# Performance work log

Measured on AMD Instinct MI355X. Metric: run time of the kernel, lower is better.

## Reference

```python
import jax, jax.numpy as jnp
import numpy as np
from jax import lax

B, S, D, H, K = 2, 2048, 1024, 16, 3  # batch, seq, embed, heads, conv kernel
DEPTH = D // H


def silu(x):
    return x * jax.nn.sigmoid(x)


def sep_conv1d(x, dw, pw, b):
    """Keras SeparableConv1D, padding='same', activation=silu.
    x: [B,S,C]; dw: [K,1,C] depthwise kernel; pw: [C,F] pointwise; b: [F]."""
    C = x.shape[-1]
    y = lax.conv_general_dilated(
        x, dw, window_strides=(1,), padding='SAME',
        dimension_numbers=('NWC', 'WIO', 'NWC'), feature_group_count=C)
    y = jnp.einsum('bsc,cf->bsf', y, pw) + b
    return silu(y)


def setup_inputs() -> dict:
    key = jax.random.key(0)
    ks = jax.random.split(key, 20)
    sc = 1.0 / np.sqrt(D)
    inp = {
        'v': jax.random.normal(ks[0], (B, S, D), jnp.float32),
        'k': jax.random.normal(ks[1], (B, S, D), jnp.float32),
        'q': jax.random.normal(ks[2], (B, S, D), jnp.float32),
        'mask': jax.random.randint(ks[3], (B, 1, 1, S), 0, 2, jnp.int32),
        # Dense wq/wk/wv (SiLU)
        'wq_w': jax.random.normal(ks[4], (D, D), jnp.float32) * sc,
        'wq_b': jnp.zeros((D,), jnp.float32),
        'wk_w': jax.random.normal(ks[5], (D, D), jnp.float32) * sc,
        'wk_b': jnp.zeros((D,), jnp.float32),
        'wv_w': jax.random.normal(ks[6], (D, D), jnp.float32) * sc,
        'wv_b': jnp.zeros((D,), jnp.float32),
        # SeparableConv1D params (depthwise [K,1,D], pointwise [D,D], bias [D])
        'dwq': jax.random.normal(ks[7], (K, 1, D), jnp.float32) * 0.1,
        'pwq': jax.random.normal(ks[8], (D, D), jnp.float32) * sc,
        'bq': jnp.zeros((D,), jnp.float32),
        'dwk': jax.random.normal(ks[9], (K, 1, D), jnp.float32) * 0.1,
        'pwk': jax.random.normal(ks[10], (D, D), jnp.float32) * sc,
        'bk': jnp.zeros((D,), jnp.float32),
        'dwv': jax.random.normal(ks[11], (K, 1, D), jnp.float32) * 0.1,
        'pwv': jax.random.normal(ks[12], (D, D), jnp.float32) * sc,
        'bv': jnp.zeros((D,), jnp.float32),
        # output Dense (SiLU)
        'wo_w': jax.random.normal(ks[13], (D, D), jnp.float32) * sc,
        'wo_b': jnp.zeros((D,), jnp.float32),
    }
    return inp


def reference(v, k, q, mask, wq_w, wq_b, wk_w, wk_b, wv_w, wv_b,
              dwq, pwq, bq, dwk, pwk, bk, dwv, pwv, bv, wo_w, wo_b):
    # Dense projections with SiLU
    qp = silu(q @ wq_w + wq_b)
    kp = silu(k @ wk_w + wk_b)
    vp = silu(v @ wv_w + wv_b)
    # SeparableConv1D enhancements (SiLU)
    qc = sep_conv1d(qp, dwq, pwq, bq)
    kc = sep_conv1d(kp, dwk, pwk, bk)
    vc = sep_conv1d(vp, dwv, pwv, bv)
    # split heads -> [B,H,S,depth]
    def split(x):
        return x.reshape(B, S, H, DEPTH).transpose(0, 2, 1, 3)
    qh, kh, vh = split(qc), split(kc), split(vc)
    # scaled dot-product attention with additive mask penalty
    logits = jnp.einsum('bhqd,bhkd->bhqk', qh, kh) / jnp.sqrt(jnp.float32(DEPTH))
    logits = logits + mask.astype(jnp.float32) * -1e9
    attn = jax.nn.softmax(logits, axis=-1)
    out = jnp.einsum('bhqk,bhkd->bhqd', attn, vh)
    out = out.transpose(0, 2, 1, 3).reshape(B, S, D)
    return silu(out @ wo_w + wo_b)
```

## Files before the change

kernel.cpp:

```cpp
#include <hip/hip_runtime.h>
#include <hip/hip_fp16.h>
#include <math.h>

#define BB 2
#define SS 2048
#define DD 1024
#define HH 16
#define MTOT (BB*SS)

typedef _Float16 f16;
typedef _Float16 f16x4 __attribute__((ext_vector_type(4)));
typedef _Float16 f16x8 __attribute__((ext_vector_type(8)));
typedef float    f32x4 __attribute__((ext_vector_type(4)));

#define KSCALE 0.1803368801111204f

__device__ __forceinline__ float silu_f(float x) {
    return x / (1.0f + __expf(-x));
}

__device__ __forceinline__ void gload16(void* lds, const void* g) {
    __builtin_amdgcn_global_load_lds(
        (const __attribute__((address_space(1))) unsigned*)g,
        (__attribute__((address_space(3))) unsigned*)lds, 16, 0, 0);
}

__global__ __launch_bounds__(256) void prep(
    const float* __restrict__ q, const float* __restrict__ k, const float* __restrict__ v,
    f16* __restrict__ x0, f16* __restrict__ x1, f16* __restrict__ x2,
    const float* __restrict__ w0, const float* __restrict__ w1, const float* __restrict__ w2,
    const float* __restrict__ w3, const float* __restrict__ w4, const float* __restrict__ w5,
    const float* __restrict__ w6, f16* __restrict__ wt,
    const int* __restrict__ mask, int* __restrict__ uidx, int* __restrict__ ucnt)
{
    __shared__ float ts[64][65];
    const int gid = blockIdx.x;
    const int t = threadIdx.x;

    if (gid < 6144) {
        const int z = gid >> 11;
        const float* src = z == 0 ? q : z == 1 ? k : v;
        f16* dst = z == 0 ? x0 : z == 1 ? x1 : x2;
        const size_t i8 = ((size_t)(gid & 2047) * 256 + t) * 8;
        const float4 a = *(const float4*)(src + i8);
        const float4 b = *(const float4*)(src + i8 + 4);
        f16x8 h = {(f16)a.x,(f16)a.y,(f16)a.z,(f16)a.w,(f16)b.x,(f16)b.y,(f16)b.z,(f16)b.w};
        *(f16x8*)(dst + i8) = h;
    } else if (gid < 7936) {
        const int w = gid - 6144;
        const int z = w >> 8;
        const int rem = w & 255;
        const int bn = (rem & 15) << 6, bk = (rem >> 4) << 6;
        const float* src;
        switch (z) {
            case 0: src = w0; break; case 1: src = w1; break;
            case 2: src = w2; break; case 3: src = w3; break;
            case 4: src = w4; break; case 5: src = w5; break;
            default: src = w6; break;
        }
        f16* dst = wt + ((size_t)z << 20);
        #pragma unroll
        for (int i = 0; i < 4; ++i) {
            const int fid = t + (i << 8);
            const int r = fid >> 4, c4 = (fid & 15) << 2;
            const float4 v4 = *(const float4*)(src + (size_t)(bk + r) * 1024 + bn + c4);
            ts[r][c4 + 0] = v4.x; ts[r][c4 + 1] = v4.y;
            ts[r][c4 + 2] = v4.z; ts[r][c4 + 3] = v4.w;
        }
        __syncthreads();
        #pragma unroll
        for (int i = 0; i < 4; ++i) {
            const int fid = t + (i << 8);
            const int nr = fid >> 4, k4 = (fid & 15) << 2;
            f16x4 h = { (f16)ts[k4 + 0][nr], (f16)ts[k4 + 1][nr],
                        (f16)ts[k4 + 2][nr], (f16)ts[k4 + 3][nr] };
            *(f16x4*)(dst + (size_t)(bn + nr) * 1024 + bk + k4) = h;
        }
    } else {
        int* ps = (int*)ts;
        const int b = gid - 7936;
        int f[8]; int cnt = 0;
        const int base = b * SS + t * 8;
        #pragma unroll
        for (int j = 0; j < 8; ++j) { f[j] = (mask[base + j] == 0); cnt += f[j]; }
        ps[t] = cnt;
        __syncthreads();
        for (int off = 1; off < 256; off <<= 1) {
            const int pv = (t >= off) ? ps[t - off] : 0;
            __syncthreads();
            ps[t] += pv;
            __syncthreads();
        }
        int pos = ps[t] - cnt;
        #pragma unroll
        for (int j = 0; j < 8; ++j)
            if (f[j]) uidx[b * SS + pos++] = t * 8 + j;
        const int total = ps[255];
        const int pad = (total + 63) & ~63;
        for (int j = total + t; j < pad; j += 256) uidx[b * SS + j] = 0;
        if (t == 0) { ucnt[b * 2] = total; ucnt[b * 2 + 1] = pad; }
    }
}

__global__ __launch_bounds__(256) void dwconv3g(
    const f16* __restrict__ p0, const f16* __restrict__ p1, const f16* __restrict__ p2,
    const float* __restrict__ w0, const float* __restrict__ w1, const float* __restrict__ w2,
    f16* __restrict__ o0, f16* __restrict__ o1, f16* __restrict__ o2)
{
    const int z = blockIdx.y;
    const f16* x = z == 0 ? p0 : z == 1 ? p1 : p2;
    const float* dw = z == 0 ? w0 : z == 1 ? w1 : w2;
    f16* y = z == 0 ? o0 : z == 1 ? o1 : o2;
    const size_t i8 = ((size_t)blockIdx.x * 256 + threadIdx.x) * 8;
    const int c = (int)(i8 % DD);
    const int s = (int)((i8 / DD) % SS);
    const f16x8 xc = *(const f16x8*)(x + i8);
    float acc[8];
    #pragma unroll
    for (int j = 0; j < 8; ++j) acc[j] = (float)xc[j] * dw[DD + c + j];
    if (s > 0) {
        const f16x8 xm = *(const f16x8*)(x + i8 - DD);
        #pragma unroll
        for (int j = 0; j < 8; ++j) acc[j] = fmaf((float)xm[j], dw[c + j], acc[j]);
    }
    if (s < SS - 1) {
        const f16x8 xp = *(const f16x8*)(x + i8 + DD);
        #pragma unroll
        for (int j = 0; j < 8; ++j) acc[j] = fmaf((float)xp[j], dw[2 * DD + c + j], acc[j]);
    }
    f16x8 o;
    #pragma unroll
    for (int j = 0; j < 8; ++j) o[j] = (f16)acc[j];
    *(f16x8*)(y + i8) = o;
}

struct GArg { const f16* A; const f16* W; const float* b; void* C; float scale; };

template<int OUTF32>
__global__ __launch_bounds__(256) void gemm_f16(GArg g0, GArg g1, GArg g2)
{
    __shared__ f16 As[128 * 64];
    __shared__ f16 Bs[128 * 64];

    const GArg ga = blockIdx.z == 0 ? g0 : blockIdx.z == 1 ? g1 : g2;
    const int t = threadIdx.x, l = t & 63, wv = t >> 6;
    const int lr = l & 15, lg = l >> 4;
    const int wr = wv >> 1, wc = wv & 1;

    const int bid = blockIdx.y * 8 + blockIdx.x;
    const int sw = (bid & 7) * 32 + (bid >> 3);
    const int brow = (sw >> 3) << 7, bcol = (sw & 7) << 7;

    const int srow = l >> 3;
    const int schk = (l & 7) ^ (l >> 3);
    const f16* Abase = ga.A + (size_t)(brow + wv * 32 + srow) * 1024 + schk * 8;
    const f16* Bbase = ga.W + (size_t)(bcol + wv * 32 + srow) * 1024 + schk * 8;

    f32x4 acc[4][4];
    #pragma unroll
    for (int m = 0; m < 4; ++m)
        #pragma unroll
        for (int n = 0; n < 4; ++n) acc[m][n] = (f32x4){0.f, 0.f, 0.f, 0.f};

    for (int kt = 0; kt < 16; ++kt) {
        const int k0 = kt << 6;
        #pragma unroll
        for (int j = 0; j < 4; ++j) {
            gload16(As + (wv * 4 + j) * 512, Abase + (size_t)j * 8 * 1024 + k0);
            gload16(Bs + (wv * 4 + j) * 512, Bbase + (size_t)j * 8 * 1024 + k0);
        }
        __syncthreads();

        #pragma unroll
        for (int kk = 0; kk < 2; ++kk) {
            f16x8 af[4], bf[4];
            #pragma unroll
            for (int m = 0; m < 4; ++m) {
                const int row = (wr << 6) + (m << 4) + lr;
                const int off = row * 128 + ((((kk << 6) | (lg << 4))) ^ ((lr & 7) << 4));
                af[m] = *(const f16x8*)((const char*)As + off);
            }
            #pragma unroll
            for (int n = 0; n < 4; ++n) {
                const int row = (wc << 6) + (n << 4) + lr;
                const int off = row * 128 + ((((kk << 6) | (lg << 4))) ^ ((lr & 7) << 4));
                bf[n] = *(const f16x8*)((const char*)Bs + off);
            }
            #pragma unroll
            for (int m = 0; m < 4; ++m)
                #pragma unroll
                for (int n = 0; n < 4; ++n)
                    acc[m][n] = __builtin_amdgcn_mfma_f32_16x16x32_f16(af[m], bf[n], acc[m][n], 0, 0, 0);
        }
        __syncthreads();
    }

    float bv[4];
    #pragma unroll
    for (int n = 0; n < 4; ++n) bv[n] = ga.b[bcol + (wc << 6) + (n << 4) + lr];
    #pragma unroll
    for (int m = 0; m < 4; ++m)
        #pragma unroll
        for (int n = 0; n < 4; ++n)
            #pragma unroll
            for (int i = 0; i < 4; ++i) {
                const int row = brow + (wr << 6) + (m << 4) + (lg << 2) + i;
                const int col = bcol + (wc << 6) + (n << 4) + lr;
                const float o = silu_f(acc[m][n][i] + bv[n]) * ga.scale;
                if (OUTF32) ((float*)ga.C)[(size_t)row * 1024 + col] = o;
                else        ((f16*)ga.C)[(size_t)row * 1024 + col] = (f16)o;
            }
}

__global__ __launch_bounds__(512) void gemm256(GArg g0, GArg g1, GArg g2)
{
    __shared__ f16 As[256 * 64];
    __shared__ f16 Bs[128 * 64];

    const GArg ga = blockIdx.z == 0 ? g0 : blockIdx.z == 1 ? g1 : g2;
    const int t = threadIdx.x, l = t & 63, wv = t >> 6;
    const int lr = l & 15, lg = l >> 4;
    const int wm = wv >> 1, wn = wv & 1;

    const int bid = blockIdx.y * 8 + blockIdx.x;
    const int sw = (bid & 7) * 16 + (bid >> 3);
    const int brow = (sw >> 3) << 8;
    const int bcol = (sw & 7) << 7;

    const int srow = l >> 3;
    const int schk = (l & 7) ^ (l >> 3);
    const f16* Abase = ga.A + (size_t)(brow + wv * 32 + srow) * 1024 + schk * 8;
    const f16* Bbase = ga.W + (size_t)(bcol + wv * 16 + srow) * 1024 + schk * 8;

    f32x4 acc[4][4];
    #pragma unroll
    for (int m = 0; m < 4; ++m)
        #pragma unroll
        for (int n = 0; n < 4; ++n) acc[m][n] = (f32x4){0.f, 0.f, 0.f, 0.f};

    for (int kt = 0; kt < 16; ++kt) {
        const int k0 = kt << 6;
        #pragma unroll
        for (int j = 0; j < 4; ++j)
            gload16(As + (wv * 4 + j) * 512, Abase + (size_t)j * 8 * 1024 + k0);
        #pragma unroll
        for (int j = 0; j < 2; ++j)
            gload16(Bs + (wv * 2 + j) * 512, Bbase + (size_t)j * 8 * 1024 + k0);
        __syncthreads();

        #pragma unroll
        for (int kk = 0; kk < 2; ++kk) {
            f16x8 af[4], bf[4];
            #pragma unroll
            for (int m = 0; m < 4; ++m) {
                const int row = (wm << 6) + (m << 4) + lr;
                const int off = row * 128 + ((((kk << 6) | (lg << 4))) ^ ((lr & 7) << 4));
                af[m] = *(const f16x8*)((const char*)As + off);
            }
            #pragma unroll
            for (int n = 0; n < 4; ++n) {
                const int row = (wn << 6) + (n << 4) + lr;
                const int off = row * 128 + ((((kk << 6) | (lg << 4))) ^ ((lr & 7) << 4));
                bf[n] = *(const f16x8*)((const char*)Bs + off);
            }
            #pragma unroll
            for (int m = 0; m < 4; ++m)
                #pragma unroll
                for (int n = 0; n < 4; ++n)
                    acc[m][n] = __builtin_amdgcn_mfma_f32_16x16x32_f16(af[m], bf[n], acc[m][n], 0, 0, 0);
        }
        __syncthreads();
    }

    float bv[4];
    #pragma unroll
    for (int n = 0; n < 4; ++n) bv[n] = ga.b[bcol + (wn << 6) + (n << 4) + lr];
    #pragma unroll
    for (int m = 0; m < 4; ++m)
        #pragma unroll
        for (int n = 0; n < 4; ++n)
            #pragma unroll
            for (int i = 0; i < 4; ++i) {
                const int row = brow + (wm << 6) + (m << 4) + (lg << 2) + i;
                const int col = bcol + (wn << 6) + (n << 4) + lr;
                const float o = silu_f(acc[m][n][i] + bv[n]) * ga.scale;
                ((f16*)ga.C)[(size_t)row * 1024 + col] = (f16)o;
            }
}

__global__ __launch_bounds__(512) void attn_f16(
    const f16* __restrict__ Q, const f16* __restrict__ Kf,
    const f16* __restrict__ Vf, const int* __restrict__ uidx,
    const int* __restrict__ ucnt, f16* __restrict__ O)
{
    __shared__ f16 Ks[2 * 64 * 64];
    __shared__ f16 Vt[2 * 64 * 64];
    __shared__ f16 Pw[8 * 16 * 64];
    __shared__ int uix[2048];

    const int t = threadIdx.x;
    const int l = t & 63, wv = t >> 6;
    const int lr = l & 15, lg = l >> 4;

    const int bid = blockIdx.x;
    const int sw = (bid & 7) * 64 + (bid >> 3);
    const int qb = (sw & 15) << 7;
    const int h  = (sw >> 4) & 15;
    const int b  = sw >> 8;

    const int cnt = ucnt[b * 2];
    const int pad = ucnt[b * 2 + 1];

    const int srow = l >> 3;
    const int schk = (l & 7) ^ (l >> 3);

    const int bkv = (t & 15) << 2;
    const int bnv = (t >> 4) << 2;

    for (int j = t; j < 2048; j += 512) uix[j] = uidx[b * SS + j];

    const size_t bbase = (size_t)b * SS;
    const size_t qrow = bbase + qb + (wv << 4) + lr;
    const f16x8 aq0 = *(const f16x8*)(Q + qrow * DD + h * 64 + (lg << 3));
    const f16x8 aq1 = *(const f16x8*)(Q + qrow * DD + h * 64 + 32 + (lg << 3));

    float m_i[4], l_i[4];
    f32x4 acc[4];
    #pragma unroll
    for (int i = 0; i < 4; ++i) { m_i[i] = -1e30f; l_i[i] = 0.f; }
    #pragma unroll
    for (int n = 0; n < 4; ++n) acc[n] = (f32x4){0.f, 0.f, 0.f, 0.f};

    const int rdswz = (lr & 7) << 4;
    const int poff = (wv << 11) + lr * 128;

    __syncthreads();

#define PROCESS(TB, KT) do {                                                  \
    const int kb = (TB) * 8192;                                               \
    f16x8 bk0[4], bk1[4];                                                     \
    _Pragma("unroll")                                                         \
    for (int n = 0; n < 4; ++n) {                                             \
        const int row = (n << 4) + lr;                                        \
        bk0[n] = *(const f16x8*)((const char*)Ks + kb + row * 128 + (((lg << 4)) ^ rdswz));        \
        bk1[n] = *(const f16x8*)((const char*)Ks + kb + row * 128 + (((64) | (lg << 4)) ^ rdswz)); \
    }                                                                         \
    const bool full = ((KT) + 64 <= cnt);                                     \
    f32x4 s[4];                                                               \
    __builtin_amdgcn_s_setprio(1);                                            \
    _Pragma("unroll")                                                         \
    for (int n = 0; n < 4; ++n) {                                             \
        f32x4 z = (f32x4){0.f, 0.f, 0.f, 0.f};                                \
        z = __builtin_amdgcn_mfma_f32_16x16x32_f16(aq0, bk0[n], z, 0, 0, 0);  \
        z = __builtin_amdgcn_mfma_f32_16x16x32_f16(aq1, bk1[n], z, 0, 0, 0);  \
        if (full) {                                                           \
            _Pragma("unroll")                                                 \
            for (int i = 0; i < 4; ++i) s[n][i] = z[i];                       \
        } else {                                                              \
            const bool valid = ((KT) + (n << 4) + lr) < cnt;                  \
            _Pragma("unroll")                                                 \
            for (int i = 0; i < 4; ++i) s[n][i] = valid ? z[i] : -1e30f;      \
        }                                                                     \
    }                                                                         \
    __builtin_amdgcn_s_setprio(0);                                            \
    float pm[4];                                                              \
    _Pragma("unroll")                                                         \
    for (int i = 0; i < 4; ++i)                                               \
        pm[i] = fmaxf(fmaxf(s[0][i], s[1][i]), fmaxf(s[2][i], s[3][i]));      \
    float g = pm[0] - m_i[0];                                                 \
    _Pragma("unroll")                                                         \
    for (int i = 1; i < 4; ++i) g = fmaxf(g, pm[i] - m_i[i]);                 \
    if (!__all(g <= 8.0f)) {                 \
        float sc[4];                                                          \
        _Pragma("unroll")                                                     \
        for (int i = 0; i < 4; ++i) {                                         \
            float pr = pm[i];                                                 \
            pr = fmaxf(pr, __shfl_xor(pr, 1));                                \
            pr = fmaxf(pr, __shfl_xor(pr, 2));                                \
            pr = fmaxf(pr, __shfl_xor(pr, 4));                                \
            pr = fmaxf(pr, __shfl_xor(pr, 8));                                \
            const float mn = fmaxf(m_i[i], pr);                               \
            sc[i] = exp2f(m_i[i] - mn);                                       \
            m_i[i] = mn;                                                      \
            l_i[i] *= sc[i];                                                  \
        }                                                                     \
        _Pragma("unroll")                                                     \
        for (int n = 0; n < 4; ++n)                                           \
            _Pragma("unroll")                                                 \
            for (int i = 0; i < 4; ++i) acc[n][i] *= sc[i];                   \
    }                                                                         \
    _Pragma("unroll")                                                         \
    for (int n = 0; n < 4; ++n)                                               \
        _Pragma("unroll")                                                     \
        for (int i = 0; i < 4; ++i) {                                         \
            const float p = exp2f(s[n][i] - m_i[i]);      \
            l_i[i] += p;                                                      \
            const int row = (lg << 2) + i;                                    \
            const int off = (wv << 11) + row * 128 +                          \
                            ((((n << 4) + lr) * 2) ^ ((row & 7) << 4));       \
            *(f16*)((char*)Pw + off) = (f16)p;                                \
        }                                                                     \
    {                                                                         \
        const f16x8 pa0 = *(const f16x8*)((const char*)Pw + poff + (((lg << 4)) ^ rdswz));        \
        const f16x8 pa1 = *(const f16x8*)((const char*)Pw + poff + (((64) | (lg << 4)) ^ rdswz)); \
        __builtin_amdgcn_s_setprio(1);                                        \
        _Pragma("unroll")                                                     \
        for (int n = 0; n < 4; ++n) {                                         \
            const int row = (n << 4) + lr;                                    \
            const f16x8 bv0 = *(const f16x8*)((const char*)Vt + kb + row * 128 + (((lg << 4)) ^ rdswz));        \
            const f16x8 bv1 = *(const f16x8*)((const char*)Vt + kb + row * 128 + (((64) | (lg << 4)) ^ rdswz)); \
            acc[n] = __builtin_amdgcn_mfma_f32_16x16x32_f16(pa0, bv0, acc[n], 0, 0, 0);  \
            acc[n] = __builtin_amdgcn_mfma_f32_16x16x32_f16(pa1, bv1, acc[n], 0, 0, 0);  \
        }                                                                     \
        __builtin_amdgcn_s_setprio(0);                                        \
    }                                                                         \
} while (0)

    for (int kt = 0; kt < pad; kt += 128) {
        const bool two = (kt + 64) < pad;
        {
            const int krow0 = uix[kt + wv * 8 + srow];
            gload16(Ks + wv * 512, Kf + (bbase + krow0) * DD + h * 64 + schk * 8);
            if (two) {
                const int krow1 = uix[kt + 64 + wv * 8 + srow];
                gload16(Ks + 4096 + wv * 512, Kf + (bbase + krow1) * DD + h * 64 + schk * 8);
            }
        }
        if (t < 256) {
            const int nhalf = two ? 2 : 1;
            for (int half = 0; half < nhalf; ++half) {
                f16x4 vl[4];
                #pragma unroll
                for (int r = 0; r < 4; ++r) {
                    const int vrow = uix[kt + half * 64 + bkv + r];
                    vl[r] = *(const f16x4*)(Vf + (bbase + vrow) * DD + h * 64 + bnv);
                }
                #pragma unroll
                for (int j = 0; j < 4; ++j) {
                    f16x4 h4 = { vl[0][j], vl[1][j], vl[2][j], vl[3][j] };
                    const int row = bnv + j;
                    const int off = half * 8192 + row * 128 + ((bkv * 2) ^ ((row & 7) << 4));
                    *(f16x4*)((char*)Vt + off) = h4;
                }
            }
        }
        __syncthreads();

        PROCESS(0, kt);
        if (two) PROCESS(1, kt + 64);

        __syncthreads();
    }
#undef PROCESS

    #pragma unroll
    for (int i = 0; i < 4; ++i) {
        l_i[i] += __shfl_xor(l_i[i], 1);
        l_i[i] += __shfl_xor(l_i[i], 2);
        l_i[i] += __shfl_xor(l_i[i], 4);
        l_i[i] += __shfl_xor(l_i[i], 8);
    }
    #pragma unroll
    for (int n = 0; n < 4; ++n)
        #pragma unroll
        for (int i = 0; i < 4; ++i) {
            const size_t row = bbase + qb + (wv << 4) + (lg << 2) + i;
            O[row * DD + h * 64 + (n << 4) + lr] = (f16)(acc[n][i] / l_i[i]);
        }
}

extern "C" void kernel_launch(void* const* d_in, const int* in_sizes, int n_in,
                              void* d_out, int out_size, void* d_ws, size_t ws_size,
                              hipStream_t stream) {
    const float* v    = (const float*)d_in[0];
    const float* k    = (const float*)d_in[1];
    const float* q    = (const float*)d_in[2];
    const int*   mask = (const int*)  d_in[3];
    const float* wq_w = (const float*)d_in[4];
    const float* wq_b = (const float*)d_in[5];
    const float* wk_w = (const float*)d_in[6];
    const float* wk_b = (const float*)d_in[7];
    const float* wv_w = (const float*)d_in[8];
    const float* wv_b = (const float*)d_in[9];
    const float* dwq  = (const float*)d_in[10];
    const float* pwq  = (const float*)d_in[11];
    const float* bq   = (const float*)d_in[12];
    const float* dwk  = (const float*)d_in[13];
    const float* pwk  = (const float*)d_in[14];
    const float* bk   = (const float*)d_in[15];
    const float* dwv  = (const float*)d_in[16];
    const float* pwv  = (const float*)d_in[17];
    const float* bv   = (const float*)d_in[18];
    const float* wo_w = (const float*)d_in[19];
    const float* wo_b = (const float*)d_in[20];
    float* out = (float*)d_out;

    const size_t NE = (size_t)MTOT * DD;
    f16* wt = (f16*)d_ws;
    f16* x0 = wt + 7 * (size_t)(1 << 20);
    f16* x1 = x0 + NE;
    f16* x2 = x1 + NE;
    f16* p0 = x2 + NE;
    f16* p1 = p0 + NE;
    f16* p2 = p1 + NE;
    f16* ao = p2 + NE;
    int* uidx = (int*)(ao + NE);
    int* ucnt = uidx + MTOT;

    f16* wtq = wt,              *wtk = wt + (1u<<20), *wtv = wt + 2*(1u<<20);
    f16* wpq = wt + 3*(1u<<20), *wpk = wt + 4*(1u<<20), *wpv = wt + 5*(1u<<20);
    f16* wto = wt + 6*(1u<<20);

    prep<<<dim3(7938), 256, 0, stream>>>(q, k, v, x0, x1, x2,
        wq_w, wk_w, wv_w, pwq, pwk, pwv, wo_w, wt, mask, uidx, ucnt);
    gemm256<<<dim3(8, 16, 3), 512, 0, stream>>>(
        GArg{x0, wtq, wq_b, p0, 1.0f}, GArg{x1, wtk, wk_b, p1, 1.0f},
        GArg{x2, wtv, wv_b, p2, 1.0f});
    dwconv3g<<<dim3(2048, 3), 256, 0, stream>>>(p0, p1, p2, dwq, dwk, dwv, x0, x1, x2);
    gemm256<<<dim3(8, 16, 3), 512, 0, stream>>>(
        GArg{x0, wpq, bq, p0, 1.0f}, GArg{x1, wpk, bk, p1, KSCALE},
        GArg{x2, wpv, bv, p2, 1.0f});
    attn_f16<<<dim3(512), 512, 0, stream>>>(p0, p1, p2, uidx, ucnt, ao);
    gemm_f16<1><<<dim3(8, 32, 1), 256, 0, stream>>>(
        GArg{ao, wto, wo_b, out, 1.0f}, GArg{ao, wto, wo_b, out, 1.0f},
        GArg{ao, wto, wo_b, out, 1.0f});
}
```

Baseline: 179.9 us.

## Transpose attention MFMA operands so each lane owns one query row

Swaps the A/B operands of the QK^T and PV MFMAs so the score tile is transposed and each lane holds scores for a single query row. The online-softmax max and sum then need one scalar state per lane instead of four, and only two cross-lane shuffles instead of four per row. P is written to LDS as packed f16x4 vectors rather than scalar f16 stores, and the output is stored as f16x4 vectors. The mask validity check now varies per element rather than per lane, and the correctness of the new LDS swizzle depends on matching the read layout.

```diff
diff --git a/kernel.cpp b/kernel.cpp
--- a/kernel.cpp
+++ b/kernel.cpp
@@ -324,10 +324,8 @@
     const f16x8 aq0 = *(const f16x8*)(Q + qrow * DD + h * 64 + (lg << 3));
     const f16x8 aq1 = *(const f16x8*)(Q + qrow * DD + h * 64 + 32 + (lg << 3));
 
-    float m_i[4], l_i[4];
+    float m_s = -1e30f, l_s = 0.f;
     f32x4 acc[4];
-    #pragma unroll
-    for (int i = 0; i < 4; ++i) { m_i[i] = -1e30f; l_i[i] = 0.f; }
     #pragma unroll
     for (int n = 0; n < 4; ++n) acc[n] = (f32x4){0.f, 0.f, 0.f, 0.f};
 
@@ -346,71 +344,70 @@
         bk1[n] = *(const f16x8*)((const char*)Ks + kb + row * 128 + (((64) | (lg << 4)) ^ rdswz)); \
     }                                                                         \
     const bool full = ((KT) + 64 <= cnt);                                     \
+                 \
     f32x4 s[4];                                                               \
     __builtin_amdgcn_s_setprio(1);                                            \
     _Pragma("unroll")                                                         \
     for (int n = 0; n < 4; ++n) {                                             \
         f32x4 z = (f32x4){0.f, 0.f, 0.f, 0.f};                                \
-        z = __builtin_amdgcn_mfma_f32_16x16x32_f16(aq0, bk0[n], z, 0, 0, 0);  \
-        z = __builtin_amdgcn_mfma_f32_16x16x32_f16(aq1, bk1[n], z, 0, 0, 0);  \
+        z = __builtin_amdgcn_mfma_f32_16x16x32_f16(bk0[n], aq0, z, 0, 0, 0);  \
+        z = __builtin_amdgcn_mfma_f32_16x16x32_f16(bk1[n], aq1, z, 0, 0, 0);  \
         if (full) {                                                           \
             _Pragma("unroll")                                                 \
             for (int i = 0; i < 4; ++i) s[n][i] = z[i];                       \
         } else {                                                              \
-            const bool valid = ((KT) + (n << 4) + lr) < cnt;                  \
             _Pragma("unroll")                                                 \
-            for (int i = 0; i < 4; ++i) s[n][i] = valid ? z[i] : -1e30f;      \
+            for (int i = 0; i < 4; ++i) {                                     \
+                const bool valid = ((KT) + (n << 4) + (lg << 2) + i) < cnt;   \
+                s[n][i] = valid ? z[i] : -1e30f;                              \
+            }                                                                 \
         }                                                                     \
     }                                                                         \
     __builtin_amdgcn_s_setprio(0);                                            \
-    float pm[4];                                                              \
+                   \
+    float pm = s[0][0];                                                       \
     _Pragma("unroll")                                                         \
-    for (int i = 0; i < 4; ++i)                                               \
-        pm[i] = fmaxf(fmaxf(s[0][i], s[1][i]), fmaxf(s[2][i], s[3][i]));      \
-    float g = pm[0] - m_i[0];                                                 \
-    _Pragma("unroll")                                                         \
-    for (int i = 1; i < 4; ++i) g = fmaxf(g, pm[i] - m_i[i]);                 \
-    if (!__all(g <= 8.0f)) {                 \
-        float sc[4];                                                          \
+    for (int n = 0; n < 4; ++n)                                               \
         _Pragma("unroll")                                                     \
-        for (int i = 0; i < 4; ++i) {                                         \
-            float pr = pm[i];                                                 \
-            pr = fmaxf(pr, __shfl_xor(pr, 1));                                \
-            pr = fmaxf(pr, __shfl_xor(pr, 2));                                \
-            pr = fmaxf(pr, __shfl_xor(pr, 4));                                \
-            pr = fmaxf(pr, __shfl_xor(pr, 8));                                \
-            const float mn = fmaxf(m_i[i], pr);                               \
-            sc[i] = exp2f(m_i[i] - mn);                                       \
-            m_i[i] = mn;                                                      \
-            l_i[i] *= sc[i];                                                  \
-        }                                                                     \
+        for (int i = 0; i < 4; ++i) pm = fmaxf(pm, s[n][i]);                  \
+    if (!__all(pm - m_s <= 8.0f)) {           \
+        float pr = pm;                                                        \
+        pr = fmaxf(pr, __shfl_xor(pr, 16));                                   \
+        pr = fmaxf(pr, __shfl_xor(pr, 32));                                   \
+        const float mn = fmaxf(m_s, pr);                                      \
+        const float sc = exp2f(m_s - mn);                                     \
+        m_s = mn;                                                             \
+        l_s *= sc;                                                            \
         _Pragma("unroll")                                                     \
         for (int n = 0; n < 4; ++n)                                           \
             _Pragma("unroll")                                                 \
-            for (int i = 0; i < 4; ++i) acc[n][i] *= sc[i];                   \
+            for (int i = 0; i < 4; ++i) acc[n][i] *= sc;                      \
     }                                                                         \
+      \
     _Pragma("unroll")                                                         \
-    for (int n = 0; n < 4; ++n)                                               \
+    for (int n = 0; n < 4; ++n) {                                             \
+        f16x4 p4;                                                             \
         _Pragma("unroll")                                                     \
         for (int i = 0; i < 4; ++i) {                                         \
-            const float p = exp2f(s[n][i] - m_i[i]);      \
-            l_i[i] += p;                                                      \
-            const int row = (lg << 2) + i;                                    \
-            const int off = (wv << 11) + row * 128 +                          \
-                            ((((n << 4) + lr) * 2) ^ ((row & 7) << 4));       \
-            *(f16*)((char*)Pw + off) = (f16)p;                                \
+            const float p = exp2f(s[n][i] - m_s);         \
+            l_s += p;                                                         \
+            p4[i] = (f16)p;                                                   \
         }                                                                     \
+        const int off = poff + (((n << 5) | (lg << 3)) ^ rdswz);              \
+        *(f16x4*)((char*)Pw + off) = p4;                                      \
+    }                                                                         \
+             \
     {                                                                         \
-        const f16x8 pa0 = *(const f16x8*)((const char*)Pw + poff + (((lg << 4)) ^ rdswz));        \
-        const f16x8 pa1 = *(const f16x8*)((const char*)Pw + poff + (((64) | (lg << 4)) ^ rdswz)); \
+        const f16x8 pb0 = *(const f16x8*)((const char*)Pw + poff + (((lg << 4)) ^ rdswz));        \
+        const f16x8 pb1 = *(const f16x8*)((const char*)Pw + poff + (((64) | (lg << 4)) ^ rdswz)); \
         __builtin_amdgcn_s_setprio(1);                                        \
         _Pragma("unroll")                                                     \
         for (int n = 0; n < 4; ++n) {                                         \
             const int row = (n << 4) + lr;                                    \
-            const f16x8 bv0 = *(const f16x8*)((const char*)Vt + kb + row * 128 + (((lg << 4)) ^ rdswz));        \
-            const f16x8 bv1 = *(const f16x8*)((const char*)Vt + kb + row * 128 + (((64) | (lg << 4)) ^ rdswz)); \
-            acc[n] = __builtin_amdgcn_mfma_f32_16x16x32_f16(pa0, bv0, acc[n], 0, 0, 0);  \
-            acc[n] = __builtin_amdgcn_mfma_f32_16x16x32_f16(pa1, bv1, acc[n], 0, 0, 0);  \
+            const f16x8 av0 = *(const f16x8*)((const char*)Vt + kb + row * 128 + (((lg << 4)) ^ rdswz));        \
+            const f16x8 av1 = *(const f16x8*)((const char*)Vt + kb + row * 128 + (((64) | (lg << 4)) ^ rdswz)); \
+            acc[n] = __builtin_amdgcn_mfma_f32_16x16x32_f16(av0, pb0, acc[n], 0, 0, 0);  \
+            acc[n] = __builtin_amdgcn_mfma_f32_16x16x32_f16(av1, pb1, acc[n], 0, 0, 0);  \
         }                                                                     \
         __builtin_amdgcn_s_setprio(0);                                        \
     }                                                                         \
@@ -453,20 +450,17 @@
     }
 #undef PROCESS
 
-    #pragma unroll
-    for (int i = 0; i < 4; ++i) {
-        l_i[i] += __shfl_xor(l_i[i], 1);
-        l_i[i] += __shfl_xor(l_i[i], 2);
-        l_i[i] += __shfl_xor(l_i[i], 4);
-        l_i[i] += __shfl_xor(l_i[i], 8);
-    }
-    #pragma unroll
-    for (int n = 0; n < 4; ++n)
-        #pragma unroll
-        for (int i = 0; i < 4; ++i) {
-            const size_t row = bbase + qb + (wv << 4) + (lg << 2) + i;
-            O[row * DD + h * 64 + (n << 4) + lr] = (f16)(acc[n][i] / l_i[i]);
-        }
+    l_s += __shfl_xor(l_s, 16);
+    l_s += __shfl_xor(l_s, 32);
+    const float inv = 1.0f / l_s;
+    const size_t orow = bbase + qb + (wv << 4) + lr;
+    #pragma unroll
+    for (int n = 0; n < 4; ++n) {
+        f16x4 o4;
+        #pragma unroll
+        for (int i = 0; i < 4; ++i) o4[i] = (f16)(acc[n][i] * inv);
+        *(f16x4*)(O + orow * DD + h * 64 + (n << 4) + (lg << 2)) = o4;
+    }
 }
 
 extern "C" void kernel_launch(void* const* d_in, const int* in_sizes, int n_in,
```

New measurement: 175.8 us. 2.3% less time.
